# Performance work log

Measured on AMD Instinct MI355X. Metric: run time of the kernel, lower is better.

Reference implementation:

```python
import jax, jax.numpy as jnp
import numpy as np


def setup_inputs() -> dict:
    key = jax.random.key(0)
    k1, k2 = jax.random.split(key)
    B, H, W, C = 8, 384, 1280, 8
    U = jax.random.normal(k1, (B, H, W, C), dtype=jnp.float32)
    flo = jax.random.normal(k2, (B, H, W, 2), dtype=jnp.float32)
    return {"U": U, "flo": flo}


def _forward_warp(U, flo):
    # Faithful port of transformerFwd: bilinear forward splatting.
    B, H, W, C = U.shape
    out_h, out_w = H, W  # out_size == (H, W) as used in get_occlusion_mask_from_flow
    # normalized sampling grid in [-1, 1]
    x_s = jnp.linspace(-1.0, 1.0, out_w, dtype=jnp.float32)  # [W]
    y_s = jnp.linspace(-1.0, 1.0, out_h, dtype=jnp.float32)  # [H]
    x_t = x_s[None, None, :] + flo[..., 0] / ((out_w - 1.0) / 2.0)  # [B,H,W]
    y_t = y_s[None, :, None] + flo[..., 1] / ((out_h - 1.0) / 2.0)  # [B,H,W]
    # map back to pixel coords
    x = (x_t.reshape(-1) + 1.0) * (W - 1.0) / 2.0  # [B*H*W]
    y = (y_t.reshape(-1) + 1.0) * (H - 1.0) / 2.0
    x0 = jnp.floor(x).astype(jnp.int32)
    x1 = x0 + 1
    y0 = jnp.floor(y).astype(jnp.int32)
    y1 = y0 + 1
    x0c = jnp.clip(x0, 0, W - 1)
    x1c = jnp.clip(x1, 0, W - 1)
    y0c = jnp.clip(y0, 0, H - 1)
    y1c = jnp.clip(y1, 0, H - 1)
    # flat destination indices into [B*H*W]
    base = jnp.repeat(jnp.arange(B, dtype=jnp.int32) * (H * W), out_h * out_w)
    idx_a = base + y0c * W + x0c
    idx_b = base + y1c * W + x0c
    idx_c = base + y0c * W + x1c
    idx_d = base + y1c * W + x1c
    x0f = x0.astype(jnp.float32)
    x1f = x1.astype(jnp.float32)
    y0f = y0.astype(jnp.float32)
    y1f = y1.astype(jnp.float32)
    # bilinear weights, zeroed where the tap fell out of bounds (clamp changed it)
    wa = jnp.where((x0c == x0) & (y0c == y0), (x1f - x) * (y1f - y), 0.0)
    wb = jnp.where((x0c == x0) & (y1c == y1), (x1f - x) * (y - y0f), 0.0)
    wc = jnp.where((x1c == x1) & (y0c == y0), (x - x0f) * (y1f - y), 0.0)
    wd = jnp.where((x1c == x1) & (y1c == y1), (x - x0f) * (y - y0f), 0.0)
    im_flat = U.reshape(-1, C)  # [B*H*W, C]
    out = jnp.zeros((B * H * W, C), dtype=jnp.float32)
    out = out.at[idx_a].add(im_flat * wa[:, None])
    out = out.at[idx_b].add(im_flat * wb[:, None])
    out = out.at[idx_c].add(im_flat * wc[:, None])
    out = out.at[idx_d].add(im_flat * wd[:, None])
    return out.reshape(B, out_h, out_w, C)


def reference(U, flo):
    return _forward_warp(U, flo)
```

## Files before the change

kernel.cpp:

```cpp
#include <hip/hip_runtime.h>
#include <math.h>

constexpr int Bc = 8, Hc = 384, Wc = 1280, Cc = 8;

constexpr int TH = 16, TW = 16;
constexpr int WIN = 5;
constexpr float FMAX = 4.5f;
constexpr int RH = TH + 2 * WIN;
constexpr int RW = TW + 2 * WIN;
constexpr int NSRC = RH * RW;
constexpr int TILES_X = Wc / TW;
constexpr int TILES_Y = Hc / TH;
constexpr int BLK = 256;

__global__ __launch_bounds__(BLK) void fwd_warp_gather(
    const float* __restrict__ U, const float* __restrict__ flo,
    float* __restrict__ out)
{
    __shared__ float2 sxy[NSRC];

    int tile = blockIdx.x;
    int b  = tile / (TILES_X * TILES_Y);
    int r  = tile % (TILES_X * TILES_Y);
    int Y0 = (r / TILES_X) * TH;
    int X0 = (r % TILES_X) * TW;
    int t  = threadIdx.x;

    const float2* flo2 = reinterpret_cast<const float2*>(flo);
    const float4* u4   = reinterpret_cast<const float4*>(U);

    for (int i = t; i < NSRC; i += BLK) {
        int sy = i / RW, sx = i - sy * RW;
        int h = Y0 - WIN + sy;
        int w = X0 - WIN + sx;
        float2 v = make_float2(-1e9f, -1e9f);
        if ((unsigned)h < (unsigned)Hc && (unsigned)w < (unsigned)Wc) {
            float2 f = flo2[(b * Hc + h) * Wc + w];
            if (fabsf(f.x) <= FMAX && fabsf(f.y) <= FMAX)
                v = make_float2((float)w + f.x, (float)h + f.y);
        }
        sxy[i] = v;
    }
    __syncthreads();

    int lpy = t / TW, lpx = t - (t / TW) * TW;
    int py = Y0 + lpy, px = X0 + lpx;
    float pxf = (float)px, pyf = (float)py;
    int pixbase = (b * Hc + py) * Wc + px;

    float a0 = 0.f, a1 = 0.f, a2 = 0.f, a3 = 0.f;
    float a4 = 0.f, a5 = 0.f, a6 = 0.f, a7 = 0.f;

    for (int dy = 0; dy < 2 * WIN + 1; ++dy) {
        int rowb   = (lpy + dy) * RW + lpx;
        int rowsrc = pixbase + (dy - WIN) * Wc;
        #pragma unroll
        for (int dx = 0; dx < 2 * WIN + 1; ++dx) {
            float2 s = sxy[rowb + dx];
            float fdx = s.x - pxf;
            float fdy = s.y - pyf;
            if (fmaxf(fabsf(fdx), fabsf(fdy)) < 1.0f) {
                float wgt = (1.0f - fabsf(fdx)) * (1.0f - fabsf(fdy));
                int sidx = rowsrc + (dx - WIN);
                float4 ua = u4[(size_t)sidx * 2];
                float4 ub = u4[(size_t)sidx * 2 + 1];
                a0 += ua.x * wgt; a1 += ua.y * wgt;
                a2 += ua.z * wgt; a3 += ua.w * wgt;
                a4 += ub.x * wgt; a5 += ub.y * wgt;
                a6 += ub.z * wgt; a7 += ub.w * wgt;
            }
        }
    }

    float4 o0 = {a0, a1, a2, a3};
    float4 o1 = {a4, a5, a6, a7};
    reinterpret_cast<float4*>(out)[(size_t)pixbase * 2]     = o0;
    reinterpret_cast<float4*>(out)[(size_t)pixbase * 2 + 1] = o1;
}

__global__ __launch_bounds__(BLK) void fwd_warp_outlier(
    const float* __restrict__ U, const float* __restrict__ flo,
    float* __restrict__ out)
{
    int tid = blockIdx.x * BLK + threadIdx.x;
    int total = Bc * Hc * Wc;
    if (tid >= total) return;
    float2 f = reinterpret_cast<const float2*>(flo)[tid];
    if (fabsf(f.x) <= FMAX && fabsf(f.y) <= FMAX) return;

    int w = tid % Wc;
    int h = (tid / Wc) % Hc;
    float x = (float)w + f.x;
    float y = (float)h + f.y;
    float x0f = floorf(x), y0f = floorf(y);
    int x0 = (int)x0f, y0 = (int)y0f;
    float wx[2] = { (x0f + 1.0f) - x, x - x0f };
    float wy[2] = { (y0f + 1.0f) - y, y - y0f };

    const float4* u4 = reinterpret_cast<const float4*>(U);
    float4 ua = u4[(size_t)tid * 2];
    float4 ub = u4[(size_t)tid * 2 + 1];
    int bbase = tid - (h * Wc + w);

    #pragma unroll
    for (int j = 0; j < 2; ++j) {
        #pragma unroll
        for (int k = 0; k < 2; ++k) {
            int ty = y0 + j, tx = x0 + k;
            if ((unsigned)ty < (unsigned)Hc && (unsigned)tx < (unsigned)Wc) {
                float wgt = wx[k] * wy[j];
                if (wgt != 0.0f) {
                    float* p = out + ((size_t)(bbase + ty * Wc + tx)) * 8;
                    atomicAdd(p + 0, ua.x * wgt);
                    atomicAdd(p + 1, ua.y * wgt);
                    atomicAdd(p + 2, ua.z * wgt);
                    atomicAdd(p + 3, ua.w * wgt);
                    atomicAdd(p + 4, ub.x * wgt);
                    atomicAdd(p + 5, ub.y * wgt);
                    atomicAdd(p + 6, ub.z * wgt);
                    atomicAdd(p + 7, ub.w * wgt);
                }
            }
        }
    }
}

extern "C" void kernel_launch(void* const* d_in, const int* in_sizes, int n_in,
                              void* d_out, int out_size, void* d_ws, size_t ws_size,
                              hipStream_t stream)
{
    const float* U   = (const float*)d_in[0];
    const float* flo = (const float*)d_in[1];
    float* out = (float*)d_out;

    int grid_g = Bc * TILES_X * TILES_Y;
    fwd_warp_gather<<<grid_g, BLK, 0, stream>>>(U, flo, out);

    int grid_o = (Bc * Hc * Wc + BLK - 1) / BLK;
    fwd_warp_outlier<<<grid_o, BLK, 0, stream>>>(U, flo, out);
}
```

Before: 395.5 us.

## Shrink gather window and compact tap hits into a bitmask before accumulating

Cuts the gather search window from 11x11 to 7x7 and lowers the flow cutoff to 2.5, so fewer neighbour candidates are tested per output pixel. Pixels whose flow falls beyond the cutoff are still scattered by the atomic outlier kernel, so the result stays correct. The hit test now runs as a branch-free pass that builds a 64-bit mask, followed by a compact loop that loads U only for set bits. The shared-memory row stride is padded by one to reduce bank conflicts. The trade-off is more pixels in the atomic outlier path for normally distributed flow, which adds atomic traffic.

```diff
diff --git a/kernel.cpp b/kernel.cpp
--- a/kernel.cpp
+++ b/kernel.cpp
@@ -4,11 +4,11 @@
 constexpr int Bc = 8, Hc = 384, Wc = 1280, Cc = 8;
 
 constexpr int TH = 16, TW = 16;
-constexpr int WIN = 5;
-constexpr float FMAX = 4.5f;
+constexpr int WIN = 3;
+constexpr float FMAX = 2.5f;
 constexpr int RH = TH + 2 * WIN;
 constexpr int RW = TW + 2 * WIN;
-constexpr int NSRC = RH * RW;
+constexpr int PSTR = RW + 1;
 constexpr int TILES_X = Wc / TW;
 constexpr int TILES_Y = Hc / TH;
 constexpr int BLK = 256;
@@ -17,7 +17,7 @@
     const float* __restrict__ U, const float* __restrict__ flo,
     float* __restrict__ out)
 {
-    __shared__ float2 sxy[NSRC];
+    __shared__ float2 sxy[RH * PSTR];
 
     int tile = blockIdx.x;
     int b  = tile / (TILES_X * TILES_Y);
@@ -29,7 +29,7 @@
     const float2* flo2 = reinterpret_cast<const float2*>(flo);
     const float4* u4   = reinterpret_cast<const float4*>(U);
 
-    for (int i = t; i < NSRC; i += BLK) {
+    for (int i = t; i < RH * RW; i += BLK) {
         int sy = i / RW, sx = i - sy * RW;
         int h = Y0 - WIN + sy;
         int w = X0 - WIN + sx;
@@ -39,37 +39,43 @@
             if (fabsf(f.x) <= FMAX && fabsf(f.y) <= FMAX)
                 v = make_float2((float)w + f.x, (float)h + f.y);
         }
-        sxy[i] = v;
+        sxy[sy * PSTR + sx] = v;
     }
     __syncthreads();
 
-    int lpy = t / TW, lpx = t - (t / TW) * TW;
+    int lpy = t >> 4, lpx = t & 15;
     int py = Y0 + lpy, px = X0 + lpx;
     float pxf = (float)px, pyf = (float)py;
     int pixbase = (b * Hc + py) * Wc + px;
 
+    unsigned long long mask = 0ull;
+    #pragma unroll
+    for (int dy = 0; dy < 2 * WIN + 1; ++dy) {
+        int rb = (lpy + dy) * PSTR + lpx;
+        #pragma unroll
+        for (int dx = 0; dx < 2 * WIN + 1; ++dx) {
+            float2 s = sxy[rb + dx];
+            float m = fmaxf(fabsf(s.x - pxf), fabsf(s.y - pyf));
+            unsigned long long hit = (m < 1.0f) ? 1ull : 0ull;
+            mask |= hit << (dy * 8 + dx);
+        }
+    }
+
     float a0 = 0.f, a1 = 0.f, a2 = 0.f, a3 = 0.f;
     float a4 = 0.f, a5 = 0.f, a6 = 0.f, a7 = 0.f;
-
-    for (int dy = 0; dy < 2 * WIN + 1; ++dy) {
-        int rowb   = (lpy + dy) * RW + lpx;
-        int rowsrc = pixbase + (dy - WIN) * Wc;
-        #pragma unroll
-        for (int dx = 0; dx < 2 * WIN + 1; ++dx) {
-            float2 s = sxy[rowb + dx];
-            float fdx = s.x - pxf;
-            float fdy = s.y - pyf;
-            if (fmaxf(fabsf(fdx), fabsf(fdy)) < 1.0f) {
-                float wgt = (1.0f - fabsf(fdx)) * (1.0f - fabsf(fdy));
-                int sidx = rowsrc + (dx - WIN);
-                float4 ua = u4[(size_t)sidx * 2];
-                float4 ub = u4[(size_t)sidx * 2 + 1];
-                a0 += ua.x * wgt; a1 += ua.y * wgt;
-                a2 += ua.z * wgt; a3 += ua.w * wgt;
-                a4 += ub.x * wgt; a5 += ub.y * wgt;
-                a6 += ub.z * wgt; a7 += ub.w * wgt;
-            }
-        }
+    while (mask) {
+        int bit = __builtin_ctzll(mask);
+        mask &= mask - 1;
+        int dy = bit >> 3, dx = bit & 7;
+        float2 s = sxy[(lpy + dy) * PSTR + lpx + dx];
+        float wgt = (1.0f - fabsf(s.x - pxf)) * (1.0f - fabsf(s.y - pyf));
+        int sidx = pixbase + (dy - WIN) * Wc + (dx - WIN);
+        float4 ua = u4[(size_t)sidx * 2];
+        float4 ub = u4[(size_t)sidx * 2 + 1];
+        a0 += ua.x * wgt; a1 += ua.y * wgt;
+        a2 += ua.z * wgt; a3 += ua.w * wgt;
+        a4 += ub.x * wgt; a5 += ub.y * wgt;
+        a6 += ub.z * wgt; a7 += ub.w * wgt;
     }
 
     float4 o0 = {a0, a1, a2, a3};
```

New measurement: 452.6 us. 14.4% more time.
